# Optimization experiments

Hardware: AMD Instinct MI355X
Metric: run time of the kernel (lower is better)

Reference implementation:

```python
import jax, jax.numpy as jnp
import numpy as np
from jax.scipy.special import logsumexp

EPS_OT = 0.05      # self.eps in AttentionOT
MAX_ITER = 100     # Sinkhorn max_iter (torch early-stops; at convergence results match)


def _l2norm(x):
    # F.normalize(x, dim=-1, p=2) with eps=1e-12
    return x / jnp.maximum(jnp.linalg.norm(x, axis=-1, keepdims=True), 1e-12)


def _sinkhorn(Cmat, mu, nu, eps):
    # Cmat: (BK, M, N), mu: (BK, M), nu: (BK, N)
    log_mu = jnp.log(mu + 1e-8)
    log_nu = jnp.log(nu + 1e-8)

    def kern(u, v):
        # log Boltzmann kernel: (-C + u_i + v_j) / eps, shape (BK, M, N)
        return (-Cmat + u[..., :, None] + v[..., None, :]) / eps

    def step(carry, _):
        u, v = carry
        u = eps * (log_mu - logsumexp(kern(u, v), axis=2)) + u
        v = eps * (log_nu - logsumexp(kern(u, v), axis=1)) + v
        return (u, v), None

    u0 = jnp.zeros_like(mu)
    v0 = jnp.zeros_like(nu)
    (u, v), _ = jax.lax.scan(jax.checkpoint(step), (u0, v0), None, length=MAX_ITER)
    return jnp.exp(kern(u, v))  # transport plan T, (BK, M, N)


def setup_inputs() -> dict:
    key = jax.random.key(0)
    Nq, M, B, K, C = 64, 16, 8, 256, 512
    ks = jax.random.split(key, 8)
    s = 1.0 / np.sqrt(C)  # torch nn.Linear default init bound
    return {
        "xq": jax.random.normal(ks[0], (Nq, M, B, C), jnp.float32),
        "xk": jax.random.normal(ks[1], (B, K, C), jnp.float32),
        "xv": jax.random.normal(ks[2], (B, K, C), jnp.float32),
        "Wq": jax.random.uniform(ks[3], (C, C), jnp.float32, -s, s),
        "Wk": jax.random.uniform(ks[4], (C, C), jnp.float32, -s, s),
        "Wv": jax.random.uniform(ks[5], (C, C), jnp.float32, -s, s),
        "Wp": jax.random.uniform(ks[6], (C, C), jnp.float32, -s, s),
        "bp": jax.random.uniform(ks[7], (C,), jnp.float32, -s, s),
    }


def reference(xq, xk, xv, Wq, Wk, Wv, Wp, bp):
    Nq, M, B, C = xq.shape
    K = xk.shape[1]
    # projections (qkv_bias=False; proj has bias). dropout probs are 0 -> identity.
    q = _l2norm(xq @ Wq.T)          # (Nq, M, B, C)
    kk = _l2norm(xk @ Wk.T)         # (B, K, C)
    v = xv @ Wv.T                   # (B, K, C)
    # torch: einsum('bkc,nmbc->bnkm') then permute(0,2,3,1) -> (B,K,M,Nq)
    sim = jnp.einsum('bkc,nmbc->bkmn', kk, q).reshape(B * K, M, Nq)
    wdist = 1.0 - sim
    mu = jnp.full((B * K, M), 1.0 / M, dtype=sim.dtype)
    nu = jnp.full((B * K, Nq), 1.0 / Nq, dtype=sim.dtype)
    T = _sinkhorn(wdist, mu, nu, EPS_OT)            # (B*K, M, Nq)
    score_map = (M * Nq * sim * T).reshape(B, K, M, Nq)
    attn = T.reshape(B, K, M, Nq).transpose(3, 0, 1, 2)  # (Nq, B, K, M)
    x = jnp.einsum('nbkm,bkc->nmbc', attn, v)            # (Nq, M, B, C)
    x = x @ Wp.T + bp
    return x, score_map
```

## Files before the change

### kernel.cpp

```cpp
#include <hip/hip_runtime.h>


typedef short   short8  __attribute__((ext_vector_type(8)));
typedef float   floatx4 __attribute__((ext_vector_type(4)));

static __device__ __forceinline__ float fastrcp(float x) {
    return __builtin_amdgcn_rcpf(x);
}
static __device__ __forceinline__ unsigned short f2bf(float f) {
    union { float f; unsigned u; } c; c.f = f;
    unsigned r = c.u + 0x7FFF + ((c.u >> 16) & 1);
    return (unsigned short)(r >> 16);
}
static __device__ __forceinline__ float bf2f(unsigned short h) {
    union { unsigned u; float f; } c; c.u = (unsigned)h << 16;
    return c.f;
}

#define RRI(x, C) __builtin_amdgcn_update_dpp(0, (x), (C), 0xf, 0xf, true)
#define RRF(x, C) __int_as_float(RRI(__float_as_int(x), (C)))
#define GATH16(d, s) do { d[0] = (s);                                        \
    d[1]  = RRF((s), 0x121); d[2]  = RRF((s), 0x122);                        \
    d[3]  = RRF((s), 0x123); d[4]  = RRF((s), 0x124);                        \
    d[5]  = RRF((s), 0x125); d[6]  = RRF((s), 0x126);                        \
    d[7]  = RRF((s), 0x127); d[8]  = RRF((s), 0x128);                        \
    d[9]  = RRF((s), 0x129); d[10] = RRF((s), 0x12a);                        \
    d[11] = RRF((s), 0x12b); d[12] = RRF((s), 0x12c);                        \
    d[13] = RRF((s), 0x12d); d[14] = RRF((s), 0x12e);                        \
    d[15] = RRF((s), 0x12f); } while (0)

__global__ __launch_bounds__(256) void prep(
    const float* __restrict__ xq, const float* __restrict__ xk,
    const float* __restrict__ xv, const float* __restrict__ Wq,
    const float* __restrict__ Wk, const float* __restrict__ Wv,
    const float* __restrict__ Wp,
    unsigned short* __restrict__ xqh, unsigned short* __restrict__ xql,
    unsigned short* __restrict__ xkh, unsigned short* __restrict__ xkl,
    unsigned short* __restrict__ xvb,
    unsigned short* __restrict__ wqh, unsigned short* __restrict__ wql,
    unsigned short* __restrict__ wkh, unsigned short* __restrict__ wkl,
    unsigned short* __restrict__ wvb, unsigned short* __restrict__ wpb)
{
    const int b = blockIdx.x;
    const float* src; unsigned short *dh, *dl; long base;
    if (b < 4096)      { src = xq; dh = xqh; dl = xql;     base = (long)b * 256; }
    else if (b < 5120) { src = xk; dh = xkh; dl = xkl;     base = (long)(b - 4096) * 256; }
    else if (b < 6144) { src = xv; dh = xvb; dl = nullptr; base = (long)(b - 5120) * 256; }
    else if (b < 6400) { src = Wq; dh = wqh; dl = wql;     base = (long)(b - 6144) * 256; }
    else if (b < 6656) { src = Wk; dh = wkh; dl = wkl;     base = (long)(b - 6400) * 256; }
    else if (b < 6912) { src = Wv; dh = wvb; dl = nullptr; base = (long)(b - 6656) * 256; }
    else               { src = Wp; dh = wpb; dl = nullptr; base = (long)(b - 6912) * 256; }
    const long i = base + threadIdx.x;
    float4 v = ((const float4*)src)[i];
    ushort4 h;
    h.x = f2bf(v.x); h.y = f2bf(v.y); h.z = f2bf(v.z); h.w = f2bf(v.w);
    ((ushort4*)dh)[i] = h;
    if (dl) {
        ushort4 l;
        l.x = f2bf(v.x - bf2f(h.x)); l.y = f2bf(v.y - bf2f(h.y));
        l.z = f2bf(v.z - bf2f(h.z)); l.w = f2bf(v.w - bf2f(h.w));
        ((ushort4*)dl)[i] = l;
    }
}

__global__ __launch_bounds__(256) void gemm_qkv2(
    const unsigned short* __restrict__ xqh, const unsigned short* __restrict__ xql,
    const unsigned short* __restrict__ xkh, const unsigned short* __restrict__ xkl,
    const unsigned short* __restrict__ xvb,
    const unsigned short* __restrict__ wqh, const unsigned short* __restrict__ wql,
    const unsigned short* __restrict__ wkh, const unsigned short* __restrict__ wkl,
    const unsigned short* __restrict__ wvb,
    unsigned short* __restrict__ qh, unsigned short* __restrict__ ql,
    unsigned short* __restrict__ kh, unsigned short* __restrict__ kl,
    unsigned short* __restrict__ vt)
{
    __shared__ __align__(16) short LB[20480];
    short (*Ash)[40] = (short(*)[40])(LB);
    short (*Asl)[40] = (short(*)[40])(LB + 5120);
    short (*Bsh)[40] = (short(*)[40])(LB + 10240);
    short (*Bsl)[40] = (short(*)[40])(LB + 15360);

    const int bx = blockIdx.x;
    const unsigned short *Ah, *Al, *Bh, *Bl;
    int seg, arow0;
    if (bx < 64)      { Ah = xqh; Al = xql; Bh = wqh; Bl = wql; arow0 = bx * 128;        seg = 0; }
    else if (bx < 80) { Ah = xkh; Al = xkl; Bh = wkh; Bl = wkl; arow0 = (bx - 64) * 128; seg = 1; }
    else              { Ah = xvb; Al = xvb; Bh = wvb; Bl = wvb; arow0 = (bx - 80) * 128; seg = 2; }
    const bool split = (seg != 2);

    const int tid  = threadIdx.x;
    const int lane = tid & 63, wv = tid >> 6;
    const int wr = (wv >> 1) * 64, wc = (wv & 1) * 64;
    const int j0 = blockIdx.y * 128;

    floatx4 acc[4][4];
#pragma unroll
    for (int i = 0; i < 4; i++)
#pragma unroll
        for (int j = 0; j < 4; j++) acc[i][j] = {0.f, 0.f, 0.f, 0.f};

    const int sr = tid >> 2, sch = (tid & 3) * 8;
    const int fr = lane & 15, fq = (lane >> 4) * 8;

    for (int k0 = 0; k0 < 512; k0 += 32) {
#pragma unroll
        for (int p = 0; p < 2; p++) {
            const int r = sr + p * 64;
            const long ao = (long)(arow0 + r) * 512 + k0 + sch;
            const long bo = (long)(j0 + r) * 512 + k0 + sch;
            *(short8*)&Ash[r][sch] = *(const short8*)(Ah + ao);
            *(short8*)&Bsh[r][sch] = *(const short8*)(Bh + bo);
            if (split) {
                *(short8*)&Asl[r][sch] = *(const short8*)(Al + ao);
                *(short8*)&Bsl[r][sch] = *(const short8*)(Bl + bo);
            }
        }
        __syncthreads();
        short8 ah[4], bh[4];
#pragma unroll
        for (int i = 0; i < 4; i++) ah[i] = *(const short8*)&Ash[wr + i * 16 + fr][fq];
#pragma unroll
        for (int j = 0; j < 4; j++) bh[j] = *(const short8*)&Bsh[wc + j * 16 + fr][fq];
        if (split) {
            short8 al[4], bl[4];
#pragma unroll
            for (int i = 0; i < 4; i++) al[i] = *(const short8*)&Asl[wr + i * 16 + fr][fq];
#pragma unroll
            for (int j = 0; j < 4; j++) bl[j] = *(const short8*)&Bsl[wc + j * 16 + fr][fq];
#pragma unroll
            for (int i = 0; i < 4; i++)
#pragma unroll
                for (int j = 0; j < 4; j++) {
                    acc[i][j] = __builtin_amdgcn_mfma_f32_16x16x32_bf16(ah[i], bh[j], acc[i][j], 0, 0, 0);
                    acc[i][j] = __builtin_amdgcn_mfma_f32_16x16x32_bf16(ah[i], bl[j], acc[i][j], 0, 0, 0);
                    acc[i][j] = __builtin_amdgcn_mfma_f32_16x16x32_bf16(al[i], bh[j], acc[i][j], 0, 0, 0);
                }
        } else {
#pragma unroll
            for (int i = 0; i < 4; i++)
#pragma unroll
                for (int j = 0; j < 4; j++)
                    acc[i][j] = __builtin_amdgcn_mfma_f32_16x16x32_bf16(ah[i], bh[j], acc[i][j], 0, 0, 0);
        }
        __syncthreads();
    }

    const int cr = (lane >> 4) * 4, cc = lane & 15;
    if (seg == 2) {
        short (*S2)[136] = (short(*)[136])LB;
#pragma unroll
        for (int i = 0; i < 4; i++)
#pragma unroll
            for (int j = 0; j < 4; j++)
#pragma unroll
                for (int r = 0; r < 4; r++)
                    S2[wc + j * 16 + cc][wr + i * 16 + cr + r] =
                        (short)f2bf(acc[i][j][r]);
        __syncthreads();
        const int orow = tid >> 1;
        const int os   = (tid & 1) * 64;
        unsigned short* dst = vt + (long)(arow0 >> 8) * 131072
                            + (long)(j0 + orow) * 256 + (arow0 & 255) + os;
#pragma unroll
        for (int c8 = 0; c8 < 8; c8++)
            *(short8*)(dst + c8 * 8) = *(const short8*)&S2[orow][os + c8 * 8];
    } else {
#pragma unroll
        for (int i = 0; i < 4; i++)
#pragma unroll
            for (int j = 0; j < 4; j++) {
                const int gj = j0 + wc + j * 16 + cc;
#pragma unroll
                for (int r = 0; r < 4; r++) {
                    const int gi = arow0 + wr + i * 16 + cr + r;
                    const float v = acc[i][j][r];
                    const unsigned short h = f2bf(v);
                    const unsigned short lo = f2bf(v - bf2f(h));
                    if (seg == 0) {
                        const long orow = (long)((gi & 7) * 1024 + ((gi >> 3) & 15) * 64 + (gi >> 7));
                        qh[orow * 512 + gj] = h;
                        ql[orow * 512 + gj] = lo;
                    } else {
                        kh[(long)gi * 512 + gj] = h;
                        kl[(long)gi * 512 + gj] = lo;
                    }
                }
            }
    }
}

__global__ __launch_bounds__(256) void gemm_sim64(
    const short* __restrict__ Ah, const short* __restrict__ Al,
    const short* __restrict__ Bh, const short* __restrict__ Bl,
    float* __restrict__ Out, const float* __restrict__ rs)
{
    const int z = blockIdx.z;
    Ah += (long)z * 131072;  Al += (long)z * 131072;
    Bh += (long)z * 524288;  Bl += (long)z * 524288;
    Out += (long)z * 262144;
    const float* rsq = rs + (long)z * 1024;
    const float* rsk = rs + 8192 + (long)z * 256;

    __shared__ __align__(16) short Ash[64][40];
    __shared__ __align__(16) short Asl[64][40];
    __shared__ __align__(16) short Bsh[64][40];
    __shared__ __align__(16) short Bsl[64][40];

    const int tid  = threadIdx.x;
    const int lane = tid & 63, wv = tid >> 6;
    const int wr = (wv >> 1) * 32, wc = (wv & 1) * 32;
    const int i0 = blockIdx.x * 64, j0 = blockIdx.y * 64;

    floatx4 acc[2][2];
#pragma unroll
    for (int i = 0; i < 2; i++)
#pragma unroll
        for (int j = 0; j < 2; j++) acc[i][j] = {0.f, 0.f, 0.f, 0.f};

    const int sr = tid >> 2, sch = (tid & 3) * 8;
    const int fr = lane & 15, fq = (lane >> 4) * 8;

    for (int k0 = 0; k0 < 512; k0 += 32) {
        const long ao = (long)(i0 + sr) * 512 + k0 + sch;
        const long bo = (long)(j0 + sr) * 512 + k0 + sch;
        *(short8*)&Ash[sr][sch] = *(const short8*)(Ah + ao);
        *(short8*)&Asl[sr][sch] = *(const short8*)(Al + ao);
        *(short8*)&Bsh[sr][sch] = *(const short8*)(Bh + bo);
        *(short8*)&Bsl[sr][sch] = *(const short8*)(Bl + bo);
        __syncthreads();
        short8 ah[2], al[2], bh[2], bl[2];
#pragma unroll
        for (int i = 0; i < 2; i++) {
            ah[i] = *(const short8*)&Ash[wr + i * 16 + fr][fq];
            al[i] = *(const short8*)&Asl[wr + i * 16 + fr][fq];
        }
#pragma unroll
        for (int j = 0; j < 2; j++) {
            bh[j] = *(const short8*)&Bsh[wc + j * 16 + fr][fq];
            bl[j] = *(const short8*)&Bsl[wc + j * 16 + fr][fq];
        }
#pragma unroll
        for (int i = 0; i < 2; i++)
#pragma unroll
            for (int j = 0; j < 2; j++) {
                acc[i][j] = __builtin_amdgcn_mfma_f32_16x16x32_bf16(ah[i], bh[j], acc[i][j], 0, 0, 0);
                acc[i][j] = __builtin_amdgcn_mfma_f32_16x16x32_bf16(ah[i], bl[j], acc[i][j], 0, 0, 0);
                acc[i][j] = __builtin_amdgcn_mfma_f32_16x16x32_bf16(al[i], bh[j], acc[i][j], 0, 0, 0);
            }
        __syncthreads();
    }

    const int cr = (lane >> 4) * 4, cc = lane & 15;
#pragma unroll
    for (int i = 0; i < 2; i++)
#pragma unroll
        for (int j = 0; j < 2; j++) {
            const int gj = j0 + wc + j * 16 + cc;
            const float sq = rsq[gj];
#pragma unroll
            for (int r = 0; r < 4; r++) {
                const int gi = i0 + wr + i * 16 + cr + r;
                Out[(long)gi * 1024 + gj] = acc[i][j][r] * rsk[gi] * sq;
            }
        }
}

template <bool BIAS, bool OPERM, bool OUT_BF16>
__global__ __launch_bounds__(256) void gemm_bf16(
    const short* __restrict__ A, const short* __restrict__ B,
    const float* __restrict__ bias, void* __restrict__ OutV,
    int Kdim, int lda, int ldb, int ldo, long sA, long sB, long sO)
{
    __shared__ __align__(16) short As[128][40];
    __shared__ __align__(16) short Bs[128][40];

    const int tid  = threadIdx.x;
    const int lane = tid & 63, wv = tid >> 6;
    const int wr = (wv >> 1) * 64, wc = (wv & 1) * 64;
    const int i0 = blockIdx.x * 128, j0 = blockIdx.y * 128;

    floatx4 acc[4][4];
#pragma unroll
    for (int i = 0; i < 4; i++)
#pragma unroll
        for (int j = 0; j < 4; j++) acc[i][j] = {0.f, 0.f, 0.f, 0.f};

    const int sr = tid >> 2, sk = (tid & 3) * 8;
    const int fr = lane & 15, fq = (lane >> 4) * 8;
    const short* pa = A + (long)blockIdx.z * sA;
    const short* pb = B + (long)blockIdx.z * sB;

    for (int k0 = 0; k0 < Kdim; k0 += 32) {
#pragma unroll
        for (int p = 0; p < 2; p++) {
            *(short8*)&As[sr + p * 64][sk] =
                *(const short8*)(pa + (long)(i0 + sr + p * 64) * lda + k0 + sk);
            *(short8*)&Bs[sr + p * 64][sk] =
                *(const short8*)(pb + (long)(j0 + sr + p * 64) * ldb + k0 + sk);
        }
        __syncthreads();
        short8 af[4], bf[4];
#pragma unroll
        for (int i = 0; i < 4; i++) af[i] = *(const short8*)&As[wr + i * 16 + fr][fq];
#pragma unroll
        for (int j = 0; j < 4; j++) bf[j] = *(const short8*)&Bs[wc + j * 16 + fr][fq];
#pragma unroll
        for (int i = 0; i < 4; i++)
#pragma unroll
            for (int j = 0; j < 4; j++)
                acc[i][j] = __builtin_amdgcn_mfma_f32_16x16x32_bf16(af[i], bf[j], acc[i][j], 0, 0, 0);
        __syncthreads();
    }

    float* Of = nullptr; unsigned short* Ob = nullptr;
    if constexpr (OUT_BF16) Ob = (unsigned short*)OutV + (long)blockIdx.z * sO;
    else                    Of = (float*)OutV + (long)blockIdx.z * sO;
    const int cr = (lane >> 4) * 4, cc = lane & 15;
#pragma unroll
    for (int i = 0; i < 4; i++) {
#pragma unroll
        for (int j = 0; j < 4; j++) {
            const int gj = j0 + wc + j * 16 + cc;
            float bb = 0.0f;
            if constexpr (BIAS) bb = bias[gj];
#pragma unroll
            for (int r = 0; r < 4; r++) {
                const int gi = i0 + wr + i * 16 + cr + r;
                float v = acc[i][j][r] + bb;
                long idx;
                if constexpr (OPERM)
                    idx = (long)((gi & 63) * 128 + ((gi >> 6) & 15) * 8 + (gi >> 10)) * ldo + gj;
                else
                    idx = (long)gi * ldo + gj;
                if constexpr (OUT_BF16) Ob[idx] = f2bf(v);
                else                    Of[idx] = v;
            }
        }
    }
}

__global__ __launch_bounds__(256) void rownorm(
    const unsigned short* __restrict__ qh, const unsigned short* __restrict__ ql,
    const unsigned short* __restrict__ kh, const unsigned short* __restrict__ kl,
    float* __restrict__ rs)
{
    const int row  = blockIdx.x * 4 + (threadIdx.x >> 6);
    const int lane = threadIdx.x & 63;
    const unsigned short *ph, *pl;
    long r;
    if (row < 8192) { ph = qh; pl = ql; r = row; }
    else            { ph = kh; pl = kl; r = row - 8192; }
    const long o = r * 512 + lane * 8;
    ushort4 h0 = *(const ushort4*)(ph + o), h1 = *(const ushort4*)(ph + o + 4);
    ushort4 l0 = *(const ushort4*)(pl + o), l1 = *(const ushort4*)(pl + o + 4);
    float ss = 0.0f;
    const unsigned short hv[8] = {h0.x, h0.y, h0.z, h0.w, h1.x, h1.y, h1.z, h1.w};
    const unsigned short lv[8] = {l0.x, l0.y, l0.z, l0.w, l1.x, l1.y, l1.z, l1.w};
#pragma unroll
    for (int i = 0; i < 8; i++) {
        const float v = bf2f(hv[i]) + bf2f(lv[i]);
        ss = fmaf(v, v, ss);
    }
#pragma unroll
    for (int off = 32; off; off >>= 1) ss += __shfl_xor(ss, off, 64);
    if (lane == 0) rs[row] = 1.0f / fmaxf(sqrtf(ss), 1e-12f);
}

__global__ __launch_bounds__(256) void sinkhorn5(
    const float* __restrict__ sim, float* __restrict__ score,
    unsigned short* __restrict__ Tt)
{
    const int lane = threadIdx.x & 63;
    const int bk   = blockIdx.x * 4 + (threadIdx.x >> 6);
    const float* S = sim + (long)bk * 1024;
    const int m = lane & 15, g = lane >> 4;

    int idx[16];
    idx[0] = m;
    idx[1]  = RRI(m, 0x121); idx[2]  = RRI(m, 0x122); idx[3]  = RRI(m, 0x123);
    idx[4]  = RRI(m, 0x124); idx[5]  = RRI(m, 0x125); idx[6]  = RRI(m, 0x126);
    idx[7]  = RRI(m, 0x127); idx[8]  = RRI(m, 0x128); idx[9]  = RRI(m, 0x129);
    idx[10] = RRI(m, 0x12a); idx[11] = RRI(m, 0x12b); idx[12] = RRI(m, 0x12c);
    idx[13] = RRI(m, 0x12d); idx[14] = RRI(m, 0x12e); idx[15] = RRI(m, 0x12f);

    float K1[16], K2R[16], sv[16];
#pragma unroll
    for (int j = 0; j < 16; j++) {
        K1[j] = __expf((S[m * 64 + g * 16 + idx[j]] - 1.0f) * 20.0f);
        const float s_ = S[idx[j] * 64 + lane];
        sv[j]  = s_;
        K2R[j] = __expf((s_ - 1.0f) * 20.0f);
    }

    const float muP = 0.0625f + 1e-8f;
    const float nuP = 0.015625f + 1e-8f;
    float b = 1.0f;
    float aB[16], bB[16];
#pragma unroll
    for (int j = 0; j < 16; j++) bB[j] = 1.0f;

#pragma unroll 1
    for (int it = 0; it < 100; it++) {
        float s0 = 0, s1 = 0, s2 = 0, s3 = 0;
#pragma unroll
        for (int j = 0; j < 4; j++) {
            s0 = fmaf(K1[j],      bB[j],      s0);
            s1 = fmaf(K1[4 + j],  bB[4 + j],  s1);
            s2 = fmaf(K1[8 + j],  bB[8 + j],  s2);
            s3 = fmaf(K1[12 + j], bB[12 + j], s3);
        }
        float s = (s0 + s1) + (s2 + s3);
        s += __shfl_xor(s, 16, 64);
        s += __shfl_xor(s, 32, 64);
        const float a = muP * fastrcp(s);
        GATH16(aB, a);
        float t0 = 0, t1 = 0, t2 = 0, t3 = 0;
#pragma unroll
        for (int j = 0; j < 4; j++) {
            t0 = fmaf(K2R[j],      aB[j],      t0);
            t1 = fmaf(K2R[4 + j],  aB[4 + j],  t1);
            t2 = fmaf(K2R[8 + j],  aB[8 + j],  t2);
            t3 = fmaf(K2R[12 + j], aB[12 + j], t3);
        }
        b = nuP * fastrcp((t0 + t1) + (t2 + t3));
        GATH16(bB, b);
    }

    float* Sc = score + (long)bk * 1024;
    unsigned short* Tp = Tt + (long)(bk >> 8) * 262144 + (bk & 255);
#pragma unroll
    for (int j = 0; j < 16; j++) {
        const int row = idx[j];
        const float Tv = aB[j] * K2R[j] * b;
        Sc[row * 64 + lane] = 1024.0f * sv[j] * Tv;
        Tp[(long)(row * 64 + lane) * 256] = f2bf(Tv);
    }
}

extern "C" void kernel_launch(void* const* d_in, const int* in_sizes, int n_in,
                              void* d_out, int out_size, void* d_ws, size_t ws_size,
                              hipStream_t stream)
{
    (void)in_sizes; (void)n_in; (void)out_size; (void)ws_size;
    const float* xq = (const float*)d_in[0];
    const float* xk = (const float*)d_in[1];
    const float* xv = (const float*)d_in[2];
    const float* Wq = (const float*)d_in[3];
    const float* Wk = (const float*)d_in[4];
    const float* Wv = (const float*)d_in[5];
    const float* Wp = (const float*)d_in[6];
    const float* bp = (const float*)d_in[7];

    float* out_x     = (float*)d_out;
    float* out_score = out_x + 8192L * 512;

    char* W = (char*)d_ws;
    const long MB = 1 << 20;
    unsigned short* qh   = (unsigned short*)(W + 0);
    unsigned short* ql   = (unsigned short*)(W + 8 * MB);
    unsigned short* xq_h = (unsigned short*)(W + 16 * MB);
    float*          simb = (float*)(W + 16 * MB);
    unsigned short* xq_l = (unsigned short*)(W + 24 * MB);
    unsigned short* xpre = (unsigned short*)(W + 24 * MB);
    unsigned short* xk_h = (unsigned short*)(W + 32 * MB);
    unsigned short* xk_l = (unsigned short*)(W + 34 * MB);
    unsigned short* Tt   = (unsigned short*)(W + 32 * MB);
    unsigned short* xv_b = (unsigned short*)(W + 36 * MB);
    unsigned short* kh   = (unsigned short*)(W + 38 * MB);
    unsigned short* kl   = (unsigned short*)(W + 40 * MB);
    unsigned short* vt   = (unsigned short*)(W + 42 * MB);
    unsigned short* wqh  = (unsigned short*)(W + 44 * MB);
    unsigned short* wql  = (unsigned short*)(W + 44 * MB + 1 * 524288);
    unsigned short* wkh  = (unsigned short*)(W + 44 * MB + 2 * 524288);
    unsigned short* wkl  = (unsigned short*)(W + 44 * MB + 3 * 524288);
    unsigned short* wvb  = (unsigned short*)(W + 44 * MB + 4 * 524288);
    unsigned short* wpb  = (unsigned short*)(W + 44 * MB + 5 * 524288);
    float*          rs   = (float*)(W + 47 * MB);

    const dim3 blk(256);

    prep<<<7168, blk, 0, stream>>>(xq, xk, xv, Wq, Wk, Wv, Wp,
                                   xq_h, xq_l, xk_h, xk_l, xv_b,
                                   wqh, wql, wkh, wkl, wvb, wpb);

    gemm_qkv2<<<dim3(96, 4), blk, 0, stream>>>(
        xq_h, xq_l, xk_h, xk_l, xv_b, wqh, wql, wkh, wkl, wvb,
        qh, ql, kh, kl, vt);

    rownorm<<<2560, blk, 0, stream>>>(qh, ql, kh, kl, rs);

    gemm_sim64<<<dim3(4, 16, 8), blk, 0, stream>>>(
        (const short*)kh, (const short*)kl, (const short*)qh, (const short*)ql,
        simb, rs);

    sinkhorn5<<<512, blk, 0, stream>>>(simb, out_score, Tt);

    gemm_bf16<false, false, true><<<dim3(8, 4, 8), blk, 0, stream>>>(
        (const short*)Tt, (const short*)vt, nullptr, xpre,
        256, 256, 256, 512, 262144, 131072, 524288);

    gemm_bf16<true, true, false><<<dim3(64, 4), blk, 0, stream>>>(
        (const short*)xpre, (const short*)wpb, bp, out_x,
        512, 512, 512, 512, 0, 0, 0);
}
```

Before: 219.6 us.

## Add Sinkhorn early exit, permlane swap reductions, and occupancy hint

```diff
diff --git a/kernel.cpp b/kernel.cpp
--- a/kernel.cpp
+++ b/kernel.cpp
@@ -3,6 +3,7 @@
 
 typedef short   short8  __attribute__((ext_vector_type(8)));
 typedef float   floatx4 __attribute__((ext_vector_type(4)));
+typedef unsigned int uint2e __attribute__((ext_vector_type(2)));
 
 static __device__ __forceinline__ float fastrcp(float x) {
     return __builtin_amdgcn_rcpf(x);
@@ -16,6 +17,29 @@
     union { unsigned u; float f; } c; c.u = (unsigned)h << 16;
     return c.f;
 }
+
+#if __has_builtin(__builtin_amdgcn_permlane16_swap)
+static __device__ __forceinline__ float xadd16(float s) {
+    uint2e r = __builtin_amdgcn_permlane16_swap(
+        __float_as_uint(s), __float_as_uint(s), false, false);
+    return __uint_as_float(r.x) + __uint_as_float(r.y);
+}
+#else
+static __device__ __forceinline__ float xadd16(float s) {
+    return s + __shfl_xor(s, 16, 64);
+}
+#endif
+#if __has_builtin(__builtin_amdgcn_permlane32_swap)
+static __device__ __forceinline__ float xadd32(float s) {
+    uint2e r = __builtin_amdgcn_permlane32_swap(
+        __float_as_uint(s), __float_as_uint(s), false, false);
+    return __uint_as_float(r.x) + __uint_as_float(r.y);
+}
+#else
+static __device__ __forceinline__ float xadd32(float s) {
+    return s + __shfl_xor(s, 32, 64);
+}
+#endif
 
 #define RRI(x, C) __builtin_amdgcn_update_dpp(0, (x), (C), 0xf, 0xf, true)
 #define RRF(x, C) __int_as_float(RRI(__float_as_int(x), (C)))
@@ -366,7 +390,7 @@
     if (lane == 0) rs[row] = 1.0f / fmaxf(sqrtf(ss), 1e-12f);
 }
 
-__global__ __launch_bounds__(256) void sinkhorn5(
+__global__ __launch_bounds__(256, 2) void sinkhorn5(
     const float* __restrict__ sim, float* __restrict__ score,
     unsigned short* __restrict__ Tt)
 {
@@ -410,8 +434,8 @@
             s3 = fmaf(K1[12 + j], bB[12 + j], s3);
         }
         float s = (s0 + s1) + (s2 + s3);
-        s += __shfl_xor(s, 16, 64);
-        s += __shfl_xor(s, 32, 64);
+        s = xadd16(s);
+        s = xadd32(s);
         const float a = muP * fastrcp(s);
         GATH16(aB, a);
         float t0 = 0, t1 = 0, t2 = 0, t3 = 0;
@@ -422,8 +446,11 @@
             t2 = fmaf(K2R[8 + j],  aB[8 + j],  t2);
             t3 = fmaf(K2R[12 + j], aB[12 + j], t3);
         }
+        const float bp_ = b;
         b = nuP * fastrcp((t0 + t1) + (t2 + t3));
         GATH16(bB, b);
+        const int conv = __builtin_fabsf(b - bp_) <= 1e-5f * __builtin_fabsf(b);
+        if (__all(conv)) break;
     }
 
     float* Sc = score + (long)bk * 1024;
```

Measured after the change: 197.0 us. 10.3% less time.
